# Kernel optimization log

Measured on AMD Instinct MI355X. Metric: run time of the kernel, lower is better.

Reference implementation:

```python
import jax, jax.numpy as jnp
import numpy as np

B, N, E = 16, 50000, 1600000  # batch, num_nodes (excl. ground), num_edges


def setup_inputs() -> dict:
    key = jax.random.key(0)
    k1, k2, k3, k4 = jax.random.split(key, 4)
    x = jax.random.normal(k1, (B, N), dtype=jnp.float32)
    # node indices in [0, N]; index 0 is the ground node prepended in forward
    src_node = jax.random.randint(k2, (E,), 0, N + 1)
    des_node = jax.random.randint(k3, (E,), 0, N + 1)
    # per-edge device params (a, w, b), gauss init std=0.01 per _init_model_param
    param = jax.random.normal(k4, (3, E), dtype=jnp.float32) * 0.01
    t = jnp.zeros((1,), dtype=jnp.float32)
    return {"t": t, "x": x, "param": param, "src_node": src_node, "des_node": des_node}


def _edge_model(param, v_s, v_d):
    # per-edge nonlinear device current: i_e = a_e * tanh(w_e*(v_s - v_d) + b_e)
    a, w, b = param[0], param[1], param[2]
    return a * jnp.tanh(w * (v_s - v_d) + b)  # (B, E)


def reference(t, x, param, src_node, des_node):
    # prepend ground node (voltage 0) -> aux_v: (B, N+1)
    aux_v = jnp.concatenate([jnp.zeros_like(x[..., :1]), x], axis=-1)
    v_s = aux_v[:, src_node]  # gather (B, E)
    v_d = aux_v[:, des_node]  # gather (B, E)
    state_i = _edge_model(param, v_s, v_d)  # (B, E)
    # KCL: current leaves src, enters des; scatter_add along node axis
    res = jnp.zeros_like(aux_v)
    res = res.at[:, src_node].add(-state_i)
    res = res.at[:, des_node].add(state_i)
    return res[:, 1:]  # drop ground node
```

## Files before the change

### kernel.cpp

```cpp
#include <hip/hip_runtime.h>

#define BATCH 16
#define PS 49
#define NPART 1024
#define SB 256
#define TPB 1024
#define LDSCAP 3840

static __device__ __forceinline__ float fast_tanh(float z) {
    float ez = __expf(2.0f * z);
    return 1.0f - 2.0f * __builtin_amdgcn_rcpf(ez + 1.0f);
}

__global__ void build_aux_T(const float* __restrict__ x, float* __restrict__ auxT, int n) {
    int idx = blockIdx.x * blockDim.x + threadIdx.x;
    if (idx >= BATCH * n) return;
    int b = idx / n;
    int i = idx % n;
    auxT[(i + 1) * BATCH + b] = x[idx];
    if (idx < BATCH) auxT[idx] = 0.0f;
}

__global__ __launch_bounds__(TPB)
void hist1(const int* __restrict__ src, const int* __restrict__ des,
           unsigned* __restrict__ blockHist, int E) {
    __shared__ unsigned h[NPART];
    int tid = threadIdx.x;
    for (int i = tid; i < NPART; i += TPB) h[i] = 0;
    __syncthreads();
    long t = (long)blockIdx.x * TPB + tid;
    long stride = (long)gridDim.x * TPB * 4;
    for (long e0 = t * 4; e0 < E; e0 += stride) {
        int ne = (int)min((long)4, (long)E - e0);
        int ss[4], dd[4];
        if (ne == 4) {
            int4 sv = *(const int4*)(src + e0);
            int4 dv = *(const int4*)(des + e0);
            ss[0]=sv.x; ss[1]=sv.y; ss[2]=sv.z; ss[3]=sv.w;
            dd[0]=dv.x; dd[1]=dv.y; dd[2]=dv.z; dd[3]=dv.w;
        } else {
            for (int j = 0; j < ne; ++j) { ss[j] = src[e0+j]; dd[j] = des[e0+j]; }
        }
        for (int j = 0; j < ne; ++j) {
            atomicAdd(&h[ss[j] / PS], 1u);
            atomicAdd(&h[dd[j] / PS], 1u);
        }
    }
    __syncthreads();
    for (int i = tid; i < NPART; i += TPB)
        blockHist[(size_t)blockIdx.x * NPART + i] = h[i];
}

__global__ __launch_bounds__(TPB)
void totals_k(const unsigned* __restrict__ blockHist, unsigned* __restrict__ binTotal) {
    int tid = threadIdx.x;
    int bin = blockIdx.x * 64 + (tid >> 4);
    int j = tid & 15;
    unsigned s = 0;
    for (int r = j; r < SB; r += 16) s += blockHist[(size_t)r * NPART + bin];
#pragma unroll
    for (int m = 1; m < 16; m <<= 1) s += __shfl_xor(s, m, 64);
    if (j == 0) binTotal[bin] = s;
}

__global__ __launch_bounds__(TPB)
void scan_bins(const unsigned* __restrict__ binTotal, unsigned* __restrict__ partStart) {
    __shared__ unsigned wsum[16];
    int tid = threadIdx.x;
    int lane = tid & 63, wv = tid >> 6;
    unsigned v = binTotal[tid];
    unsigned inc = v;
    for (int off = 1; off < 64; off <<= 1) {
        unsigned t = __shfl_up(inc, off, 64);
        if (lane >= off) inc += t;
    }
    if (lane == 63) wsum[wv] = inc;
    __syncthreads();
    if (tid < 16) {
        unsigned w = wsum[tid], winc = w;
        for (int off = 1; off < 16; off <<= 1) {
            unsigned t = __shfl_up(winc, off, 64);
            if (tid >= off) winc += t;
        }
        wsum[tid] = winc - w;
    }
    __syncthreads();
    unsigned excl = (inc - v) + wsum[wv];
    partStart[tid] = excl;
    if (tid == TPB - 1) partStart[NPART] = excl + v;
}

__global__ __launch_bounds__(TPB)
void offs_k(unsigned* __restrict__ blockHist, const unsigned* __restrict__ partStart) {
    int tid = threadIdx.x;
    int binLocal = tid >> 4;
    int bin = blockIdx.x * 64 + binLocal;
    int j = tid & 15;
    const int per = SB / 16;
    unsigned ls = 0;
    for (int r = j * per; r < (j + 1) * per; ++r)
        ls += blockHist[(size_t)r * NPART + bin];
    int waveBase = (binLocal & 3) * 16;
    unsigned excl = 0;
    for (int k = 0; k < 16; ++k) {
        unsigned v = __shfl(ls, waveBase + k, 64);
        if (k < j) excl += v;
    }
    unsigned run = partStart[bin] + excl;
    for (int r = j * per; r < (j + 1) * per; ++r) {
        unsigned tmp = blockHist[(size_t)r * NPART + bin];
        blockHist[(size_t)r * NPART + bin] = run;
        run += tmp;
    }
}

__global__ __launch_bounds__(TPB)
void scatter1(const int* __restrict__ src, const int* __restrict__ des,
              const float* __restrict__ param, const unsigned* __restrict__ offsets,
              uint4* __restrict__ bins, int E) {
    __shared__ unsigned offs[NPART];
    int tid = threadIdx.x;
    for (int i = tid; i < NPART; i += TPB)
        offs[i] = offsets[(size_t)blockIdx.x * NPART + i];
    __syncthreads();
    long t = (long)blockIdx.x * TPB + tid;
    long stride = (long)gridDim.x * TPB * 4;
    for (long e0 = t * 4; e0 < E; e0 += stride) {
        int ne = (int)min((long)4, (long)E - e0);
        int ss[4], dd[4];
        float aa[4], ww[4], cc[4];
        if (ne == 4) {
            int4 sv = *(const int4*)(src + e0);
            int4 dv = *(const int4*)(des + e0);
            float4 av = *(const float4*)(param + e0);
            float4 wv = *(const float4*)(param + E + e0);
            float4 cv = *(const float4*)(param + 2 * (size_t)E + e0);
            ss[0]=sv.x; ss[1]=sv.y; ss[2]=sv.z; ss[3]=sv.w;
            dd[0]=dv.x; dd[1]=dv.y; dd[2]=dv.z; dd[3]=dv.w;
            aa[0]=av.x; aa[1]=av.y; aa[2]=av.z; aa[3]=av.w;
            ww[0]=wv.x; ww[1]=wv.y; ww[2]=wv.z; ww[3]=wv.w;
            cc[0]=cv.x; cc[1]=cv.y; cc[2]=cv.z; cc[3]=cv.w;
        } else {
            for (int j = 0; j < ne; ++j) {
                ss[j] = src[e0+j]; dd[j] = des[e0+j];
                aa[j] = param[e0+j]; ww[j] = param[E + e0 + j];
                cc[j] = param[2 * (size_t)E + e0 + j];
            }
        }
        for (int j = 0; j < ne; ++j) {
            int s = ss[j], d = dd[j];
            unsigned slot = atomicAdd(&offs[s / PS], 1u);
            bins[slot] = make_uint4((unsigned)s | ((unsigned)d << 16),
                                    __float_as_uint(-aa[j]), __float_as_uint(ww[j]),
                                    __float_as_uint(cc[j]));
            unsigned slot2 = atomicAdd(&offs[d / PS], 1u);
            bins[slot2] = make_uint4((unsigned)d | ((unsigned)s << 16),
                                     __float_as_uint(aa[j]), __float_as_uint(-ww[j]),
                                     __float_as_uint(cc[j]));
        }
    }
}

__global__ __launch_bounds__(TPB)
void sort_accumulate(const uint4* __restrict__ bins, const unsigned* __restrict__ partStart,
                     const float* __restrict__ auxT, float* __restrict__ outT, int n) {
    extern __shared__ uint4 srec[];
    unsigned* bump = (unsigned*)(srec + LDSCAP);
    unsigned* ns   = bump + PS;
    int p = blockIdx.x;
    int tid = threadIdx.x;
    unsigned lo = partStart[p], hi = partStart[p + 1];
    unsigned cnt = hi - lo;
    unsigned cl = cnt < (unsigned)LDSCAP ? cnt : (unsigned)LDSCAP;
    int base = p * PS;

    for (int i = tid; i < PS; i += TPB) bump[i] = 0;
    __syncthreads();
    const unsigned* keys = (const unsigned*)bins;
    for (unsigned k = tid; k < cl; k += TPB) {
        unsigned o = keys[(size_t)(lo + k) * 4] & 0xFFFFu;
        atomicAdd(&bump[o - (unsigned)base], 1u);
    }
    __syncthreads();
    if (tid == 0) {
        unsigned run = 0;
        for (int i = 0; i < PS; ++i) {
            unsigned c = bump[i];
            ns[i] = run;
            bump[i] = run;
            run += c;
        }
        ns[PS] = run;
    }
    __syncthreads();
    for (unsigned k = tid; k < cl; k += TPB) {
        uint4 rec = bins[lo + k];
        unsigned slot = atomicAdd(&bump[(rec.x & 0xFFFFu) - (unsigned)base], 1u);
        srec[slot] = rec;
    }
    __syncthreads();
    int lane = tid & 63;
    int wv = tid >> 6;
    int ri = lane >> 2, lj = lane & 3;
    const float4* aux4 = (const float4*)auxT;
    float4* out4 = (float4*)outT;
    for (int nl = wv; nl < PS; nl += TPB / 64) {
        int node = base + nl;
        if (node == 0 || node > n) continue;
        unsigned l2 = ns[nl], h2 = ns[nl + 1];
        float4 vo = aux4[(size_t)node * 4 + lj];
        float ax = 0.0f, ay = 0.0f, az = 0.0f, as_ = 0.0f;
        for (unsigned kk = l2; kk < h2; kk += 16) {
            unsigned k = kk + (unsigned)ri;
            uint4 rec;
            if (k < h2) rec = srec[k];
            else { rec.x = 0u; rec.y = 0u; rec.z = 0u; rec.w = 0u; }
            unsigned rem = rec.x >> 16;
            float4 vr = aux4[(size_t)rem * 4 + lj];
            float a = __uint_as_float(rec.y);
            float w = __uint_as_float(rec.z);
            float c = __uint_as_float(rec.w);
            ax  += a * fast_tanh(w * (vo.x - vr.x) + c);
            ay  += a * fast_tanh(w * (vo.y - vr.y) + c);
            az  += a * fast_tanh(w * (vo.z - vr.z) + c);
            as_ += a * fast_tanh(w * (vo.w - vr.w) + c);
        }
        for (unsigned kk = lo + cl; kk < hi; kk += 16) {
            unsigned k = kk + (unsigned)ri;
            uint4 rec;
            if (k < hi) rec = bins[k];
            else { rec.x = 0u; rec.y = 0u; rec.z = 0u; rec.w = 0u; }
            if ((int)(rec.x & 0xFFFFu) != node) rec.y = 0u;
            unsigned rem = rec.x >> 16;
            float4 vr = aux4[(size_t)rem * 4 + lj];
            float a = __uint_as_float(rec.y);
            float w = __uint_as_float(rec.z);
            float c = __uint_as_float(rec.w);
            ax  += a * fast_tanh(w * (vo.x - vr.x) + c);
            ay  += a * fast_tanh(w * (vo.y - vr.y) + c);
            az  += a * fast_tanh(w * (vo.z - vr.z) + c);
            as_ += a * fast_tanh(w * (vo.w - vr.w) + c);
        }
#pragma unroll
        for (int m = 4; m < 64; m <<= 1) {
            ax  += __shfl_xor(ax, m, 64);
            ay  += __shfl_xor(ay, m, 64);
            az  += __shfl_xor(az, m, 64);
            as_ += __shfl_xor(as_, m, 64);
        }
        if (lane < 4)
            out4[(size_t)node * 4 + lane] = make_float4(ax, ay, az, as_);
    }
}

__global__ void transpose_out(const float* __restrict__ outT, float* __restrict__ out, int n) {
    int idx = blockIdx.x * blockDim.x + threadIdx.x;
    if (idx >= BATCH * n) return;
    int b = idx / n;
    int j = idx % n;
    out[idx] = outT[(size_t)(j + 1) * BATCH + b];
}

__global__ void edge_direct(const float* __restrict__ param,
                            const int* __restrict__ src,
                            const int* __restrict__ des,
                            const float* __restrict__ x,
                            float* __restrict__ out, int E, int n) {
    int e = blockIdx.x * blockDim.x + threadIdx.x;
    if (e >= E) return;
    float a = param[e], w = param[E + e], c = param[2 * E + e];
    int s = src[e], d = des[e];
#pragma unroll
    for (int b = 0; b < BATCH; ++b) {
        float vs = s ? x[(size_t)b * n + (s - 1)] : 0.0f;
        float vd = d ? x[(size_t)b * n + (d - 1)] : 0.0f;
        float st = a * tanhf(w * (vs - vd) + c);
        if (s) atomicAdd(out + (size_t)b * n + (s - 1), -st);
        if (d) atomicAdd(out + (size_t)b * n + (d - 1), st);
    }
}

extern "C" void kernel_launch(void* const* d_in, const int* in_sizes, int n_in,
                              void* d_out, int out_size, void* d_ws, size_t ws_size,
                              hipStream_t stream) {
    const float* x     = (const float*)d_in[1];
    const float* param = (const float*)d_in[2];
    const int*   src   = (const int*)d_in[3];
    const int*   des   = (const int*)d_in[4];
    float* out = (float*)d_out;

    int E = in_sizes[3];
    int n = in_sizes[1] / BATCH;
    int total = BATCH * n;

    auto alignup = [](size_t v) { return (v + 255) & ~(size_t)255; };
    size_t auxBytes  = alignup((size_t)(n + 1) * BATCH * sizeof(float));
    size_t outTBytes = auxBytes;
    size_t bhBytes   = alignup((size_t)SB * NPART * sizeof(unsigned));
    size_t psBytes   = alignup((size_t)(NPART + 1) * sizeof(unsigned));
    size_t btBytes   = alignup((size_t)NPART * sizeof(unsigned));
    size_t binBytes  = alignup((size_t)2 * E * sizeof(uint4));
    size_t need      = auxBytes + outTBytes + bhBytes + psBytes + btBytes + binBytes;

    size_t saLds = (size_t)LDSCAP * sizeof(uint4) + (2 * PS + 1 + 8) * sizeof(unsigned);

    if (ws_size >= need && (n + 1) <= NPART * PS && n <= 65534) {
        char* w = (char*)d_ws;
        float*    auxT      = (float*)w;     w += auxBytes;
        float*    outT      = (float*)w;     w += outTBytes;
        unsigned* blockHist = (unsigned*)w;  w += bhBytes;
        unsigned* partStart = (unsigned*)w;  w += psBytes;
        unsigned* binTotal  = (unsigned*)w;  w += btBytes;
        uint4*    bins      = (uint4*)w;

        build_aux_T<<<(total + 255) / 256, 256, 0, stream>>>(x, auxT, n);
        hist1<<<SB, TPB, 0, stream>>>(src, des, blockHist, E);
        totals_k<<<NPART / 64, TPB, 0, stream>>>(blockHist, binTotal);
        scan_bins<<<1, TPB, 0, stream>>>(binTotal, partStart);
        offs_k<<<NPART / 64, TPB, 0, stream>>>(blockHist, partStart);
        scatter1<<<SB, TPB, 0, stream>>>(src, des, param, blockHist, bins, E);
        sort_accumulate<<<NPART, TPB, saLds, stream>>>(bins, partStart, auxT, outT, n);
        transpose_out<<<(total + 255) / 256, 256, 0, stream>>>(outT, out, n);
        return;
    }

    (void)hipMemsetAsync(out, 0, (size_t)out_size * sizeof(float), stream);
    edge_direct<<<(E + 255) / 256, 256, 0, stream>>>(param, src, des, x, out, E, n);
}
```

Before: 127.1 us.

## Fuse aux transpose into histogram, write output directly, fold tanh constants, double SB

Folds the x-to-auxT transpose into the hist1 kernel and drops the separate transpose_out kernel by writing results straight into the batch-major output from sort_accumulate. The tanh evaluation is rewritten as exp2 plus rcp with 2*log2(e) pre-folded into w and b during binning, which trims per-edge ALU work. SB doubles from 256 to 512 blocks for the histogram and scatter passes, which also doubles the per-block histogram size. The direct output stores are strided by n per batch and therefore uncoalesced.

Measured after the change: 151.3 us. +19.0%, slower.

```diff
diff --git a/kernel.cpp b/kernel.cpp
--- a/kernel.cpp
+++ b/kernel.cpp
@@ -3,30 +3,27 @@
 #define BATCH 16
 #define PS 49
 #define NPART 1024
-#define SB 256
+#define SB 512
 #define TPB 1024
 #define LDSCAP 3840
 
-static __device__ __forceinline__ float fast_tanh(float z) {
-    float ez = __expf(2.0f * z);
-    return 1.0f - 2.0f * __builtin_amdgcn_rcpf(ez + 1.0f);
-}
-
-__global__ void build_aux_T(const float* __restrict__ x, float* __restrict__ auxT, int n) {
-    int idx = blockIdx.x * blockDim.x + threadIdx.x;
-    if (idx >= BATCH * n) return;
-    int b = idx / n;
-    int i = idx % n;
-    auxT[(i + 1) * BATCH + b] = x[idx];
-    if (idx < BATCH) auxT[idx] = 0.0f;
-}
+#define TWO_LOG2E 2.8853900817779268f
+
 
 __global__ __launch_bounds__(TPB)
 void hist1(const int* __restrict__ src, const int* __restrict__ des,
-           unsigned* __restrict__ blockHist, int E) {
+           const float* __restrict__ x, float* __restrict__ auxT,
+           unsigned* __restrict__ blockHist, int E, int n) {
     __shared__ unsigned h[NPART];
     int tid = threadIdx.x;
     for (int i = tid; i < NPART; i += TPB) h[i] = 0;
+    for (long idx = (long)blockIdx.x * TPB + tid; idx < (long)BATCH * n;
+         idx += (long)gridDim.x * TPB) {
+        int b = (int)(idx / n);
+        int i = (int)(idx - (long)b * n);
+        auxT[(size_t)(i + 1) * BATCH + b] = x[idx];
+        if (idx < BATCH) auxT[idx] = 0.0f;
+    }
     __syncthreads();
     long t = (long)blockIdx.x * TPB + tid;
     long stride = (long)gridDim.x * TPB * 4;
@@ -149,29 +146,36 @@
         }
         for (int j = 0; j < ne; ++j) {
             int s = ss[j], d = dd[j];
+            float wq = ww[j] * TWO_LOG2E, cq = cc[j] * TWO_LOG2E;
             unsigned slot = atomicAdd(&offs[s / PS], 1u);
             bins[slot] = make_uint4((unsigned)s | ((unsigned)d << 16),
-                                    __float_as_uint(-aa[j]), __float_as_uint(ww[j]),
-                                    __float_as_uint(cc[j]));
+                                    __float_as_uint(-aa[j]), __float_as_uint(wq),
+                                    __float_as_uint(cq));
             unsigned slot2 = atomicAdd(&offs[d / PS], 1u);
             bins[slot2] = make_uint4((unsigned)d | ((unsigned)s << 16),
-                                     __float_as_uint(aa[j]), __float_as_uint(-ww[j]),
-                                     __float_as_uint(cc[j]));
-        }
-    }
+                                     __float_as_uint(aa[j]), __float_as_uint(-wq),
+                                     __float_as_uint(cq));
+        }
+    }
+}
+
+static __device__ __forceinline__ float edge_eval(float a, float a2, float wq, float cq,
+                                                  float dv) {
+    float ez = __builtin_amdgcn_exp2f(__builtin_fmaf(wq, dv, cq));
+    float r = __builtin_amdgcn_rcpf(ez + 1.0f);
+    return __builtin_fmaf(-a2, r, a);
 }
 
 __global__ __launch_bounds__(TPB)
 void sort_accumulate(const uint4* __restrict__ bins, const unsigned* __restrict__ partStart,
-                     const float* __restrict__ auxT, float* __restrict__ outT, int n) {
+                     const float* __restrict__ auxT, float* __restrict__ out, int n) {
     extern __shared__ uint4 srec[];
     unsigned* bump = (unsigned*)(srec + LDSCAP);
     unsigned* ns   = bump + PS;
     int p = blockIdx.x;
     int tid = threadIdx.x;
     unsigned lo = partStart[p], hi = partStart[p + 1];
-    unsigned cnt = hi - lo;
-    unsigned cl = cnt < (unsigned)LDSCAP ? cnt : (unsigned)LDSCAP;
+    unsigned cl = min(hi - lo, (unsigned)LDSCAP);
     int base = p * PS;
 
     for (int i = tid; i < PS; i += TPB) bump[i] = 0;
@@ -203,7 +207,6 @@
     int wv = tid >> 6;
     int ri = lane >> 2, lj = lane & 3;
     const float4* aux4 = (const float4*)auxT;
-    float4* out4 = (float4*)outT;
     for (int nl = wv; nl < PS; nl += TPB / 64) {
         int node = base + nl;
         if (node == 0 || node > n) continue;
@@ -218,12 +221,13 @@
             unsigned rem = rec.x >> 16;
             float4 vr = aux4[(size_t)rem * 4 + lj];
             float a = __uint_as_float(rec.y);
-            float w = __uint_as_float(rec.z);
-            float c = __uint_as_float(rec.w);
-            ax  += a * fast_tanh(w * (vo.x - vr.x) + c);
-            ay  += a * fast_tanh(w * (vo.y - vr.y) + c);
-            az  += a * fast_tanh(w * (vo.z - vr.z) + c);
-            as_ += a * fast_tanh(w * (vo.w - vr.w) + c);
+            float a2 = a + a;
+            float wq = __uint_as_float(rec.z);
+            float cq = __uint_as_float(rec.w);
+            ax  += edge_eval(a, a2, wq, cq, vo.x - vr.x);
+            ay  += edge_eval(a, a2, wq, cq, vo.y - vr.y);
+            az  += edge_eval(a, a2, wq, cq, vo.z - vr.z);
+            as_ += edge_eval(a, a2, wq, cq, vo.w - vr.w);
         }
         for (unsigned kk = lo + cl; kk < hi; kk += 16) {
             unsigned k = kk + (unsigned)ri;
@@ -234,12 +238,13 @@
             unsigned rem = rec.x >> 16;
             float4 vr = aux4[(size_t)rem * 4 + lj];
             float a = __uint_as_float(rec.y);
-            float w = __uint_as_float(rec.z);
-            float c = __uint_as_float(rec.w);
-            ax  += a * fast_tanh(w * (vo.x - vr.x) + c);
-            ay  += a * fast_tanh(w * (vo.y - vr.y) + c);
-            az  += a * fast_tanh(w * (vo.z - vr.z) + c);
-            as_ += a * fast_tanh(w * (vo.w - vr.w) + c);
+            float a2 = a + a;
+            float wq = __uint_as_float(rec.z);
+            float cq = __uint_as_float(rec.w);
+            ax  += edge_eval(a, a2, wq, cq, vo.x - vr.x);
+            ay  += edge_eval(a, a2, wq, cq, vo.y - vr.y);
+            az  += edge_eval(a, a2, wq, cq, vo.z - vr.z);
+            as_ += edge_eval(a, a2, wq, cq, vo.w - vr.w);
         }
 #pragma unroll
         for (int m = 4; m < 64; m <<= 1) {
@@ -248,17 +253,15 @@
             az  += __shfl_xor(az, m, 64);
             as_ += __shfl_xor(as_, m, 64);
         }
-        if (lane < 4)
-            out4[(size_t)node * 4 + lane] = make_float4(ax, ay, az, as_);
-    }
-}
-
-__global__ void transpose_out(const float* __restrict__ outT, float* __restrict__ out, int n) {
-    int idx = blockIdx.x * blockDim.x + threadIdx.x;
-    if (idx >= BATCH * n) return;
-    int b = idx / n;
-    int j = idx % n;
-    out[idx] = outT[(size_t)(j + 1) * BATCH + b];
+        if (lane < 4) {
+            int j = node - 1;
+            int b0 = lj * 4;
+            out[(size_t)(b0 + 0) * n + j] = ax;
+            out[(size_t)(b0 + 1) * n + j] = ay;
+            out[(size_t)(b0 + 2) * n + j] = az;
+            out[(size_t)(b0 + 3) * n + j] = as_;
+        }
+    }
 }
 
 __global__ void edge_direct(const float* __restrict__ param,
@@ -291,36 +294,31 @@
 
     int E = in_sizes[3];
     int n = in_sizes[1] / BATCH;
-    int total = BATCH * n;
 
     auto alignup = [](size_t v) { return (v + 255) & ~(size_t)255; };
     size_t auxBytes  = alignup((size_t)(n + 1) * BATCH * sizeof(float));
-    size_t outTBytes = auxBytes;
     size_t bhBytes   = alignup((size_t)SB * NPART * sizeof(unsigned));
     size_t psBytes   = alignup((size_t)(NPART + 1) * sizeof(unsigned));
     size_t btBytes   = alignup((size_t)NPART * sizeof(unsigned));
     size_t binBytes  = alignup((size_t)2 * E * sizeof(uint4));
-    size_t need      = auxBytes + outTBytes + bhBytes + psBytes + btBytes + binBytes;
+    size_t need      = auxBytes + bhBytes + psBytes + btBytes + binBytes;
 
     size_t saLds = (size_t)LDSCAP * sizeof(uint4) + (2 * PS + 1 + 8) * sizeof(unsigned);
 
     if (ws_size >= need && (n + 1) <= NPART * PS && n <= 65534) {
         char* w = (char*)d_ws;
         float*    auxT      = (float*)w;     w += auxBytes;
-        float*    outT      = (float*)w;     w += outTBytes;
         unsigned* blockHist = (unsigned*)w;  w += bhBytes;
         unsigned* partStart = (unsigned*)w;  w += psBytes;
         unsigned* binTotal  = (unsigned*)w;  w += btBytes;
         uint4*    bins      = (uint4*)w;
 
-        build_aux_T<<<(total + 255) / 256, 256, 0, stream>>>(x, auxT, n);
-        hist1<<<SB, TPB, 0, stream>>>(src, des, blockHist, E);
+        hist1<<<SB, TPB, 0, stream>>>(src, des, x, auxT, blockHist, E, n);
         totals_k<<<NPART / 64, TPB, 0, stream>>>(blockHist, binTotal);
         scan_bins<<<1, TPB, 0, stream>>>(binTotal, partStart);
         offs_k<<<NPART / 64, TPB, 0, stream>>>(blockHist, partStart);
         scatter1<<<SB, TPB, 0, stream>>>(src, des, param, blockHist, bins, E);
-        sort_accumulate<<<NPART, TPB, saLds, stream>>>(bins, partStart, auxT, outT, n);
-        transpose_out<<<(total + 255) / 256, 256, 0, stream>>>(outT, out, n);
+        sort_accumulate<<<NPART, TPB, saLds, stream>>>(bins, partStart, auxT, out, n);
         return;
     }
 
```
